# Kernel optimization log

Hardware: AMD Instinct MI355X
Metric: run time of the kernel (lower is better)

Reference implementation:

```python
import jax, jax.numpy as jnp
import numpy as np

REG_MAX = 16
TOPK = 13
ALPHA = 1.0
BETA = 6.0
MATCH_W = 0.5
IOU_W = 7.5
DFL_W = 1.5
EPS = 1e-7
NEG_INF = -1e30


def _iou(b1, b2):
    # xyxy IoU, broadcastable [..., 4]
    x1 = jnp.maximum(b1[..., 0], b2[..., 0]); y1 = jnp.maximum(b1[..., 1], b2[..., 1])
    x2 = jnp.minimum(b1[..., 2], b2[..., 2]); y2 = jnp.minimum(b1[..., 3], b2[..., 3])
    inter = jnp.maximum(x2 - x1, 0.0) * jnp.maximum(y2 - y1, 0.0)
    a1 = (b1[..., 2] - b1[..., 0]) * (b1[..., 3] - b1[..., 1])
    a2 = (b2[..., 2] - b2[..., 0]) * (b2[..., 3] - b2[..., 1])
    return inter / (a1 + a2 - inter + EPS)


def _ciou(b1, b2):
    iou = _iou(b1, b2)
    w1 = b1[..., 2] - b1[..., 0]; h1 = b1[..., 3] - b1[..., 1]
    w2 = b2[..., 2] - b2[..., 0]; h2 = b2[..., 3] - b2[..., 1]
    cw = jnp.maximum(b1[..., 2], b2[..., 2]) - jnp.minimum(b1[..., 0], b2[..., 0])
    ch = jnp.maximum(b1[..., 3], b2[..., 3]) - jnp.minimum(b1[..., 1], b2[..., 1])
    c2 = cw * cw + ch * ch + EPS
    rho2 = ((b2[..., 0] + b2[..., 2] - b1[..., 0] - b1[..., 2]) ** 2
            + (b2[..., 1] + b2[..., 3] - b1[..., 1] - b1[..., 3]) ** 2) / 4.0
    v = (4.0 / jnp.pi ** 2) * (jnp.arctan(w2 / (h2 + EPS)) - jnp.arctan(w1 / (h1 + EPS))) ** 2
    a = jax.lax.stop_gradient(v / (v - iou + (1.0 + EPS)))
    return iou - (rho2 / c2 + v * a)


def _per_sample(ps, pb, bd, gtb, gtl, vcm, anchor, stride):
    # ps [N,C], pb [N,4], bd [N,4*R], gtb [M,4], gtl [M], vcm [C] bool
    N, C = ps.shape
    M = gtb.shape[0]
    lab = jnp.clip(gtl, 0, C - 1)
    gt_valid = (gtl >= 0) & (gtl < C) & vcm[lab]
    ax, ay = anchor[:, 0], anchor[:, 1]
    inside = ((ax[None, :] >= gtb[:, 0:1]) & (ax[None, :] <= gtb[:, 2:3])
              & (ay[None, :] >= gtb[:, 1:2]) & (ay[None, :] <= gtb[:, 3:4]))  # [M,N]
    iou_mn = _iou(pb[None, :, :], gtb[:, None, :])                             # [M,N]
    cls_mn = jax.nn.sigmoid(ps[:, lab]).T                                      # [M,N]
    align = jnp.where(inside & gt_valid[:, None], cls_mn ** ALPHA * iou_mn ** BETA, NEG_INF)
    top_vals, top_idx = jax.lax.top_k(align, TOPK)                             # [M,K]
    cand = jnp.full((M, N), NEG_INF, ps.dtype).at[jnp.arange(M)[:, None], top_idx].set(top_vals)
    best = cand.max(0)          # final metric per anchor
    mg = cand.argmax(0)         # winning GT (first max == earliest GT, matching loop order)
    fg = best > -1.0            # align >= 0 always; non-candidates stay at NEG_INF
    m_lab = jnp.clip(gtl[mg], 0, C - 1)
    ov = iou_mn[mg, jnp.arange(N)]
    fgf = fg.astype(ps.dtype)
    tgt_scores = jax.nn.one_hot(m_lab, C, dtype=ps.dtype) * (jnp.maximum(ov, 0.1) * fgf)[:, None]
    tb = jnp.where(fg[:, None], gtb[mg], pb)   # safe target boxes (masked out when not fg)

    # classification BCE over valid classes (mean)
    bce = jnp.maximum(ps, 0.0) - ps * tgt_scores + jnp.log1p(jnp.exp(-jnp.abs(ps)))
    vc = vcm.astype(ps.dtype)
    match = (bce * vc[None, :]).sum() / (N * jnp.maximum(vc.sum(), 1.0))

    cnt = fg.sum()
    ciou_v = _ciou(pb, tb)
    iou_loss = jnp.where(cnt > 0, ((1.0 - ciou_v) * fgf).sum() / jnp.maximum(cnt, 1), 0.0)
    miou_sum = (_iou(pb, tb) * fgf).sum()
    probs = jax.nn.sigmoid(ps)
    pos_sum = (probs[jnp.arange(N), m_lab] * fgf).sum()

    # DFL
    d = jnp.concatenate([anchor - tb[:, :2], tb[:, 2:] - anchor], -1) / stride  # [N,4]
    d = jnp.clip(d, 0.0, REG_MAX - 1 - 0.01)
    tl = d.astype(jnp.int32)
    tr = jnp.minimum(tl + 1, REG_MAX - 1)
    wl = tr.astype(ps.dtype) - d
    wr = 1.0 - wl
    logp = jax.nn.log_softmax(bd.reshape(N, 4, REG_MAX), -1)
    ll = -jnp.take_along_axis(logp, tl[..., None], -1)[..., 0]
    lr = -jnp.take_along_axis(logp, tr[..., None], -1)[..., 0]
    dfl = jnp.where(cnt > 0, ((ll * wl + lr * wr) * fgf[:, None]).sum() / jnp.maximum(cnt * 4, 1), 0.0)

    mx = jnp.where(vcm[None, :], probs, NEG_INF).max(-1)
    neg_sum = (mx * (1.0 - fgf)).sum()
    neg_cnt = N - cnt
    return match, iou_loss, dfl, cnt, neg_cnt, pos_sum, neg_sum, miou_sum


def setup_inputs() -> dict:
    key = jax.random.key(0)
    B, N, C, M, R = 16, 8400, 80, 64, REG_MAX
    ks = jax.random.split(key, 7)
    pts, sts = [], []
    for s in (8, 16, 32):
        n = 640 // s
        g = (np.arange(n) + 0.5) * s
        xv, yv = np.meshgrid(g, g)
        pts.append(np.stack([xv.ravel(), yv.ravel()], 1))
        sts.append(np.full((n * n, 1), s, np.float32))
    anchor_points = jnp.asarray(np.concatenate(pts).astype(np.float32))  # [8400,2]
    stride_tensor = jnp.asarray(np.concatenate(sts))                      # [8400,1]
    c = anchor_points[None] + jax.random.normal(ks[0], (B, N, 2)) * stride_tensor[None]
    wh = jax.random.uniform(ks[1], (B, N, 2), minval=8.0, maxval=128.0)
    pred_boxes = jnp.concatenate([jnp.clip(c - wh / 2, 0.0, 640.0),
                                  jnp.clip(c + wh / 2, 0.0, 640.0)], -1)
    gc = jax.random.uniform(ks[2], (B, M, 2), minval=64.0, maxval=576.0)
    gwh = jax.random.uniform(ks[3], (B, M, 2), minval=16.0, maxval=128.0)
    gt_boxes = jnp.concatenate([gc - gwh / 2, gc + gwh / 2], -1)
    gt_labels = jax.random.randint(ks[4], (B, M), 0, C)
    class_mask = jnp.ones((B, C), bool)
    pred_scores = jax.random.normal(ks[5], (B, N, C))
    box_distribution = jax.random.normal(ks[6], (B, N, 4 * R))
    return {"pred_scores": pred_scores, "pred_boxes": pred_boxes,
            "anchor_points": anchor_points, "stride_tensor": stride_tensor,
            "box_distribution": box_distribution, "gt_boxes": gt_boxes,
            "gt_labels": gt_labels, "class_mask": class_mask}


def reference(pred_scores, pred_boxes, anchor_points, stride_tensor,
              box_distribution, gt_boxes, gt_labels, class_mask):
    B = pred_scores.shape[0]
    f = lambda ps, pb, bd, gtb, gtl, vcm: _per_sample(ps, pb, bd, gtb, gtl, vcm,
                                                      anchor_points, stride_tensor)
    match, iou_l, dfl, cnt, ncnt, psum, nsum, misum = jax.vmap(f)(
        pred_scores, pred_boxes, box_distribution, gt_boxes, gt_labels, class_mask)
    tot_pos = cnt.sum()
    tot_neg = ncnt.sum()
    total_match = match.sum(); total_iou = iou_l.sum(); total_dfl = dfl.sum()
    loss = (MATCH_W * total_match + IOU_W * total_iou + DFL_W * total_dfl) / B
    mean_pos = psum.sum() / jnp.maximum(tot_pos, 1)
    mean_neg = nsum.sum() / jnp.maximum(tot_neg, 1)
    mean_miou = misum.sum() / jnp.maximum(tot_pos, 1)
    return (loss, total_match / B, total_iou / B, total_dfl / B,
            tot_pos.astype(jnp.float32), mean_pos, mean_neg, mean_miou)
```

## Files before the change

kernel.cpp:

```cpp
#include <hip/hip_runtime.h>
#include <stdint.h>

#define TOPK 13
#define NEG_INF_F (-1e30f)
#define EPSF 1e-7f
#define L2EF 1.4426950408889634f
#define LN2F 0.6931471805599453f
#define MAXCAND 2048

__device__ __forceinline__ int mask_at(const uint8_t* __restrict__ raw, int i) {
    bool as_u8 = (raw[1] | raw[2] | raw[3]) != 0;
    return as_u8 ? (raw[i] != 0) : (((const int*)raw)[i] != 0);
}

__device__ __forceinline__ float iou_pair(float ax1, float ay1, float ax2, float ay2,
                                          float bx1, float by1, float bx2, float by2) {
    float x1 = fmaxf(ax1, bx1), y1 = fmaxf(ay1, by1);
    float x2 = fminf(ax2, bx2), y2 = fminf(ay2, by2);
    float inter = fmaxf(x2 - x1, 0.f) * fmaxf(y2 - y1, 0.f);
    float a1 = (ax2 - ax1) * (ay2 - ay1);
    float a2 = (bx2 - bx1) * (by2 - by1);
    return inter / (a1 + a2 - inter + EPSF);
}

__device__ __forceinline__ float sigmoid_fast(float s) {
    return 1.f / (1.f + exp2f(-s * L2EF));
}
__device__ __forceinline__ float softplus_bce(float s) {
    float t = exp2f(-fabsf(s) * L2EF);
    return fmaxf(s, 0.f) + log2f(1.f + t) * LN2F;
}

__global__ __launch_bounds__(64) void assign_grid_k(
    const float* __restrict__ ps, const float* __restrict__ pb,
    const float* __restrict__ gtb, const int* __restrict__ gtl,
    const uint8_t* __restrict__ mraw,
    unsigned long long* __restrict__ best, int B, int N, int C, int M) {
    int b = blockIdx.x % B;
    int m = blockIdx.x / B;

    int lbl = gtl[b * M + m];
    int lab = min(max(lbl, 0), C - 1);
    if (!((lbl >= 0) && (lbl < C) && (mask_at(mraw, b * C + lab) != 0))) return;

    float4 g = ((const float4*)gtb)[(size_t)b * M + m];

    const int   n0_[3]  = { 0, 6400, 8000 };
    const int   dim_[3] = { 80, 40, 20 };
    const float sv_[3]  = { 8.f, 16.f, 32.f };

    int ix0[3], iy0[3], ww[3], pre[4];
    pre[0] = 0;
#pragma unroll
    for (int l = 0; l < 3; ++l) {
        float s = sv_[l]; int d = dim_[l];
        int ax0 = max(0,     (int)ceilf (g.x / s - 0.5f));
        int ax1 = min(d - 1, (int)floorf(g.z / s - 0.5f));
        int ay0 = max(0,     (int)ceilf (g.y / s - 0.5f));
        int ay1 = min(d - 1, (int)floorf(g.w / s - 0.5f));
        int w = max(0, ax1 - ax0 + 1);
        int h = max(0, ay1 - ay0 + 1);
        ix0[l] = ax0; iy0[l] = ay0; ww[l] = w;
        pre[l + 1] = pre[l] + w * h;
    }
    int tot = pre[3];
    if (tot == 0) return;

    const float* psb = ps + (size_t)b * N * C + lab;
    const float4* pbb = (const float4*)pb + (size_t)b * N;
    int lane = threadIdx.x;

    float lv[TOPK];
    int   li[TOPK];
#pragma unroll
    for (int j = 0; j < TOPK; ++j) { lv[j] = NEG_INF_F; li[j] = -1; }

    for (int t = lane; t < tot; t += 64) {
        int l = (t >= pre[1]) + (t >= pre[2]);
        int r = t - pre[l];
        int w = ww[l];
        int iy = r / w, ix = r - iy * w;
        int gx = ix0[l] + ix, gy = iy0[l] + iy;
        int n = n0_[l] + gy * dim_[l] + gx;
        float4 p = pbb[n];
        float iou = iou_pair(p.x, p.y, p.z, p.w, g.x, g.y, g.z, g.w);
        float sc = psb[(size_t)n * C];
        float i3 = iou * iou * iou;
        float val = sigmoid_fast(sc) * i3 * i3;
        if (val > lv[TOPK - 1]) {
            bool placed = false;
#pragma unroll
            for (int j = TOPK - 1; j >= 1; --j) {
                if (!placed) {
                    if (val > lv[j - 1]) { lv[j] = lv[j - 1]; li[j] = li[j - 1]; }
                    else { lv[j] = val; li[j] = n; placed = true; }
                }
            }
            if (!placed) { lv[0] = val; li[0] = n; }
        }
    }

    unsigned key = 0xFFFFFFFFu - (unsigned)m;
    unsigned long long* bb = best + (size_t)b * N;
    int rounds = min(tot, TOPK);
    for (int p = 0; p < rounds; ++p) {
        float bv = lv[0]; int bn = li[0];
        for (int off = 32; off > 0; off >>= 1) {
            float ov = __shfl_down(bv, off, 64);
            int   on = __shfl_down(bn, off, 64);
            if (ov > bv || (ov == bv && (unsigned)on < (unsigned)bn)) { bv = ov; bn = on; }
        }
        bv = __shfl(bv, 0, 64);
        bn = __shfl(bn, 0, 64);
        if (bn < 0) break;
        if (li[0] == bn) {
            unsigned long long pk =
                ((unsigned long long)__float_as_uint(lv[0]) << 32) | (unsigned long long)key;
            atomicMax(bb + bn, pk);
#pragma unroll
            for (int j = 0; j < TOPK - 1; ++j) { lv[j] = lv[j + 1]; li[j] = li[j + 1]; }
            lv[TOPK - 1] = NEG_INF_F; li[TOPK - 1] = -1;
        }
    }
}

__global__ __launch_bounds__(256) void assign_topk_k(
    const float* __restrict__ ps, const float* __restrict__ pb,
    const float* __restrict__ anch, const float* __restrict__ gtb,
    const int* __restrict__ gtl, const uint8_t* __restrict__ mraw,
    unsigned long long* __restrict__ best, int B, int N, int C, int M) {
    int b = blockIdx.x % B;
    int m = blockIdx.x / B;

    __shared__ float cval[MAXCAND];
    __shared__ int   cidx[MAXCAND];
    __shared__ int   scnt;
    if (threadIdx.x == 0) scnt = 0;

    int lbl = gtl[b * M + m];
    int lab = min(max(lbl, 0), C - 1);
    bool valid = (lbl >= 0) && (lbl < C) && (mask_at(mraw, b * C + lab) != 0);
    __syncthreads();

    if (valid) {
        float4 g = ((const float4*)gtb)[(size_t)b * M + m];
        const float* psb = ps + (size_t)b * N * C + lab;
        const float4* pbb = (const float4*)pb + (size_t)b * N;
        for (int n = threadIdx.x; n < N; n += 256) {
            float2 a = ((const float2*)anch)[n];
            if (a.x < g.x || a.x > g.z || a.y < g.y || a.y > g.w) continue;
            float4 p = pbb[n];
            float iou = iou_pair(p.x, p.y, p.z, p.w, g.x, g.y, g.z, g.w);
            float s = psb[(size_t)n * C];
            float i3 = iou * iou * iou;
            float val = sigmoid_fast(s) * i3 * i3;
            int slot = atomicAdd(&scnt, 1);
            if (slot < MAXCAND) { cval[slot] = val; cidx[slot] = n; }
        }
    }
    __syncthreads();
    if (!valid || threadIdx.x >= 64) return;

    int total = min(scnt, MAXCAND);
    if (total == 0) return;
    int lane = threadIdx.x;

    float lv[TOPK];
    int   li[TOPK];
#pragma unroll
    for (int j = 0; j < TOPK; ++j) { lv[j] = NEG_INF_F; li[j] = -1; }
    for (int i = lane; i < total; i += 64) {
        float v = cval[i]; int ix = cidx[i];
        if (v > lv[TOPK - 1]) {
            bool placed = false;
#pragma unroll
            for (int j = TOPK - 1; j >= 1; --j) {
                if (!placed) {
                    if (v > lv[j - 1]) { lv[j] = lv[j - 1]; li[j] = li[j - 1]; }
                    else { lv[j] = v; li[j] = ix; placed = true; }
                }
            }
            if (!placed) { lv[0] = v; li[0] = ix; }
        }
    }

    unsigned key = 0xFFFFFFFFu - (unsigned)m;
    unsigned long long* bb = best + (size_t)b * N;
    int rounds = min(total, TOPK);
    for (int p = 0; p < rounds; ++p) {
        float bv = lv[0]; int bn = li[0];
        for (int off = 32; off > 0; off >>= 1) {
            float ov = __shfl_down(bv, off, 64);
            int   on = __shfl_down(bn, off, 64);
            if (ov > bv || (ov == bv && (unsigned)on < (unsigned)bn)) { bv = ov; bn = on; }
        }
        bv = __shfl(bv, 0, 64);
        bn = __shfl(bn, 0, 64);
        if (bn < 0) break;
        if (li[0] == bn) {
            unsigned long long pk =
                ((unsigned long long)__float_as_uint(lv[0]) << 32) | (unsigned long long)key;
            atomicMax(bb + bn, pk);
#pragma unroll
            for (int j = 0; j < TOPK - 1; ++j) { lv[j] = lv[j + 1]; li[j] = li[j + 1]; }
            lv[TOPK - 1] = NEG_INF_F; li[TOPK - 1] = -1;
        }
    }
}

__global__ __launch_bounds__(256, 1) void per_anchor_k(
    const float* __restrict__ ps, const float* __restrict__ pb,
    const float* __restrict__ anch, const float* __restrict__ strd,
    const float* __restrict__ bd, const float* __restrict__ gtb,
    const int* __restrict__ gtl, const uint8_t* __restrict__ mraw,
    const unsigned long long* __restrict__ best,
    float* __restrict__ partials, int B, int N, int C, int M) {
    int b = blockIdx.y;
    int n = blockIdx.x * 256 + threadIdx.x;

    __shared__ int smask[256];
    __shared__ int s_notall;
    __shared__ float sred[4 * 8];
    if (threadIdx.x == 0) s_notall = 0;
    __syncthreads();
    for (int c = threadIdx.x; c < C && c < 256; c += 256) {
        int v = mask_at(mraw, b * C + c);
        smask[c] = v;
        if (!v) s_notall = 1;
    }
    __syncthreads();
    bool allm = (s_notall == 0);

    float acc0 = 0, acc1 = 0, acc2 = 0, acc3 = 0, acc4 = 0, acc5 = 0, acc6 = 0;

    if (n < N) {
        unsigned long long pk = best[(size_t)b * N + n];
        bool fg = (pk != 0ull);
        int mg = fg ? (int)(0xFFFFFFFFu - (unsigned)(pk & 0xFFFFFFFFull)) : 0;
        int lbl = gtl[b * M + mg];
        int m_lab = min(max(lbl, 0), C - 1);

        const float* psr = ps + ((size_t)b * N + n) * C;
        float bce_sum = 0.f, smax = NEG_INF_F;

        if (C == 80 && allm) {
            const float4* p4 = (const float4*)psr;
            float4 s4[20];
#pragma unroll
            for (int i = 0; i < 20; ++i) s4[i] = p4[i];
#pragma unroll
            for (int i = 0; i < 20; ++i) {
                bce_sum += softplus_bce(s4[i].x) + softplus_bce(s4[i].y) +
                           softplus_bce(s4[i].z) + softplus_bce(s4[i].w);
                smax = fmaxf(smax, fmaxf(fmaxf(s4[i].x, s4[i].y), fmaxf(s4[i].z, s4[i].w)));
            }
        } else if (allm) {
            int c4 = C & ~3;
            for (int c = 0; c < c4; c += 4) {
                float4 s4 = *(const float4*)(psr + c);
                bce_sum += softplus_bce(s4.x) + softplus_bce(s4.y) +
                           softplus_bce(s4.z) + softplus_bce(s4.w);
                smax = fmaxf(smax, fmaxf(fmaxf(s4.x, s4.y), fmaxf(s4.z, s4.w)));
            }
            for (int c = c4; c < C; ++c) {
                float s = psr[c];
                bce_sum += softplus_bce(s);
                smax = fmaxf(smax, s);
            }
        } else {
            for (int c = 0; c < C; ++c) {
                float s = psr[c];
                if (smask[c]) { bce_sum += softplus_bce(s); smax = fmaxf(smax, s); }
            }
        }

        acc1 = fg ? 1.f : 0.f;
        acc3 = fg ? 0.f : sigmoid_fast(smax);

        if (fg) {
            const float* bdr = bd + ((size_t)b * N + n) * 64;
            const float4* bq4 = (const float4*)bdr;
            float4 bq[16];
#pragma unroll
            for (int i = 0; i < 16; ++i) bq[i] = bq4[i];
            float4 p = ((const float4*)pb)[(size_t)b * N + n];
            float4 g = ((const float4*)gtb)[(size_t)b * M + mg];
            float2 an = ((const float2*)anch)[n];
            float stv = strd[n];
            float slab = psr[m_lab];

            float ov = iou_pair(p.x, p.y, p.z, p.w, g.x, g.y, g.z, g.w);
            bce_sum -= fmaxf(ov, 0.1f) * slab;
            acc2 = sigmoid_fast(slab);
            acc4 = ov;
            float w1 = p.z - p.x, h1 = p.w - p.y;
            float w2 = g.z - g.x, h2 = g.w - g.y;
            float cw = fmaxf(p.z, g.z) - fminf(p.x, g.x);
            float ch = fmaxf(p.w, g.w) - fminf(p.y, g.y);
            float c2 = cw * cw + ch * ch + EPSF;
            float dx = g.x + g.z - p.x - p.z;
            float dy = g.y + g.w - p.y - p.w;
            float rho2 = (dx * dx + dy * dy) * 0.25f;
            const float PI = 3.14159265358979323846f;
            float dv = atanf(w2 / (h2 + EPSF)) - atanf(w1 / (h1 + EPSF));
            float v = (4.f / (PI * PI)) * dv * dv;
            float a = v / (v - ov + 1.f + EPSF);
            acc5 = 1.f - (ov - (rho2 / c2 + v * a));
            float dall[4] = { (an.x - g.x) / stv, (an.y - g.y) / stv,
                              (g.z - an.x) / stv, (g.w - an.y) / stv };
            float dfl = 0.f;
#pragma unroll
            for (int k = 0; k < 4; ++k) {
                float4 q0 = bq[k * 4 + 0], q1 = bq[k * 4 + 1];
                float4 q2 = bq[k * 4 + 2], q3 = bq[k * 4 + 3];
                float mxv = fmaxf(fmaxf(fmaxf(q0.x, q0.y), fmaxf(q0.z, q0.w)),
                                  fmaxf(fmaxf(q1.x, q1.y), fmaxf(q1.z, q1.w)));
                mxv = fmaxf(mxv, fmaxf(fmaxf(fmaxf(q2.x, q2.y), fmaxf(q2.z, q2.w)),
                                        fmaxf(fmaxf(q3.x, q3.y), fmaxf(q3.z, q3.w))));
                float se = exp2f((q0.x - mxv) * L2EF) + exp2f((q0.y - mxv) * L2EF) +
                           exp2f((q0.z - mxv) * L2EF) + exp2f((q0.w - mxv) * L2EF) +
                           exp2f((q1.x - mxv) * L2EF) + exp2f((q1.y - mxv) * L2EF) +
                           exp2f((q1.z - mxv) * L2EF) + exp2f((q1.w - mxv) * L2EF) +
                           exp2f((q2.x - mxv) * L2EF) + exp2f((q2.y - mxv) * L2EF) +
                           exp2f((q2.z - mxv) * L2EF) + exp2f((q2.w - mxv) * L2EF) +
                           exp2f((q3.x - mxv) * L2EF) + exp2f((q3.y - mxv) * L2EF) +
                           exp2f((q3.z - mxv) * L2EF) + exp2f((q3.w - mxv) * L2EF);
                float lse = mxv + log2f(se) * LN2F;
                float d = fminf(fmaxf(dall[k], 0.f), 14.99f);
                int tl = (int)d;
                int tr = min(tl + 1, 15);
                float wl = (float)tr - d;
                float xtl = bdr[k * 16 + tl];
                float xtr = bdr[k * 16 + tr];
                dfl += (lse - xtl) * wl + (lse - xtr) * (1.f - wl);
            }
            acc6 = dfl;
        }
        acc0 = bce_sum;
    }

    int lane = threadIdx.x & 63, wid = threadIdx.x >> 6;
    float accs[7] = { acc0, acc1, acc2, acc3, acc4, acc5, acc6 };
#pragma unroll
    for (int j = 0; j < 7; ++j) {
        float v = accs[j];
        for (int off = 32; off > 0; off >>= 1) v += __shfl_down(v, off, 64);
        if (lane == 0) sred[wid * 8 + j] = v;
    }
    __syncthreads();
    if (threadIdx.x < 7) {
        float s = sred[0 * 8 + threadIdx.x] + sred[1 * 8 + threadIdx.x] +
                  sred[2 * 8 + threadIdx.x] + sred[3 * 8 + threadIdx.x];
        atomicAdd(&partials[b * 8 + threadIdx.x], s);
    }
}

__global__ void finalize_k(const float* __restrict__ partials, const uint8_t* __restrict__ mraw,
                           float* __restrict__ out, int B, int N, int C) {
    int lane = threadIdx.x;
    float tm = 0, ti = 0, td = 0, tp = 0, tneg = 0, pos = 0, neg = 0, miou = 0;
    if (lane < B) {
        float vcs = 0.f;
        for (int c = 0; c < C; ++c) vcs += mask_at(mraw, lane * C + c) ? 1.f : 0.f;
        const float* pr = partials + lane * 8;
        float cnt = pr[1];
        tm = pr[0] / ((float)N * fmaxf(vcs, 1.f));
        ti = (cnt > 0.f) ? pr[5] / fmaxf(cnt, 1.f) : 0.f;
        td = (cnt > 0.f) ? pr[6] / fmaxf(cnt * 4.f, 1.f) : 0.f;
        tp = cnt; tneg = (float)N - cnt;
        pos = pr[2]; neg = pr[3]; miou = pr[4];
    }
    for (int off = 32; off > 0; off >>= 1) {
        tm += __shfl_down(tm, off, 64);   ti += __shfl_down(ti, off, 64);
        td += __shfl_down(td, off, 64);   tp += __shfl_down(tp, off, 64);
        tneg += __shfl_down(tneg, off, 64); pos += __shfl_down(pos, off, 64);
        neg += __shfl_down(neg, off, 64); miou += __shfl_down(miou, off, 64);
    }
    if (lane == 0) {
        float Bf = (float)B;
        out[0] = (0.5f * tm + 7.5f * ti + 1.5f * td) / Bf;
        out[1] = tm / Bf;
        out[2] = ti / Bf;
        out[3] = td / Bf;
        out[4] = tp;
        out[5] = pos / fmaxf(tp, 1.f);
        out[6] = neg / fmaxf(tneg, 1.f);
        out[7] = miou / fmaxf(tp, 1.f);
    }
}

extern "C" void kernel_launch(void* const* d_in, const int* in_sizes, int n_in,
                              void* d_out, int out_size, void* d_ws, size_t ws_size,
                              hipStream_t stream) {
    const float* ps   = (const float*)d_in[0];
    const float* pb   = (const float*)d_in[1];
    const float* anch = (const float*)d_in[2];
    const float* strd = (const float*)d_in[3];
    const float* bd   = (const float*)d_in[4];
    const float* gtb  = (const float*)d_in[5];
    const int*   gtl  = (const int*)d_in[6];
    const uint8_t* cmsk = (const uint8_t*)d_in[7];

    int N = in_sizes[2] / 2;
    int B = in_sizes[1] / (4 * N);
    int C = in_sizes[0] / (B * N);
    int M = in_sizes[6] / B;

    unsigned long long* best = (unsigned long long*)d_ws;
    size_t off = (size_t)B * N * sizeof(unsigned long long);
    off = (off + 255) & ~(size_t)255;
    float* partials = (float*)((char*)d_ws + off);
    size_t total = off + (size_t)B * 8 * sizeof(float);

    hipMemsetAsync(d_ws, 0, total, stream);
    if (N == 8400) {
        assign_grid_k<<<B * M, 64, 0, stream>>>(ps, pb, gtb, gtl, cmsk, best, B, N, C, M);
    } else {
        assign_topk_k<<<B * M, 256, 0, stream>>>(ps, pb, anch, gtb, gtl, cmsk, best, B, N, C, M);
    }
    dim3 gB((N + 255) / 256, B);
    per_anchor_k<<<gB, 256, 0, stream>>>(ps, pb, anch, strd, bd, gtb, gtl, cmsk, best,
                                         partials, B, N, C, M);
    finalize_k<<<1, 64, 0, stream>>>(partials, cmsk, (float*)d_out, B, N, C);
}
```

Baseline: 161.1 us.

## Overlap assignment with dense BCE pass and fold finalize into last block

For the N==8400 path, the per-GT assignment waves are packed four per 256-thread block. They run in the same launch as the dense per-anchor BCE/max pass, which does not depend on the assignment. The foreground-dependent terms move to a second kernel that reads the saved per-anchor max, and a last-block-done counter folds the finalize step into that kernel. This removes one launch and lets the assignment overlap the heavy class-score read, at the cost of an extra smax buffer round trip and a second pass over the foreground data.

```diff
diff --git a/kernel.cpp b/kernel.cpp
--- a/kernel.cpp
+++ b/kernel.cpp
@@ -31,13 +31,14 @@
     return fmaxf(s, 0.f) + log2f(1.f + t) * LN2F;
 }
 
-__global__ __launch_bounds__(64) void assign_grid_k(
+__device__ __forceinline__ void assign_wave(
     const float* __restrict__ ps, const float* __restrict__ pb,
     const float* __restrict__ gtb, const int* __restrict__ gtl,
     const uint8_t* __restrict__ mraw,
-    unsigned long long* __restrict__ best, int B, int N, int C, int M) {
-    int b = blockIdx.x % B;
-    int m = blockIdx.x / B;
+    unsigned long long* __restrict__ best, int B, int N, int C, int M,
+    int t, int lane) {
+    int b = t % B;
+    int m = t / B;
 
     int lbl = gtl[b * M + m];
     int lab = min(max(lbl, 0), C - 1);
@@ -68,16 +69,15 @@
 
     const float* psb = ps + (size_t)b * N * C + lab;
     const float4* pbb = (const float4*)pb + (size_t)b * N;
-    int lane = threadIdx.x;
 
     float lv[TOPK];
     int   li[TOPK];
 #pragma unroll
     for (int j = 0; j < TOPK; ++j) { lv[j] = NEG_INF_F; li[j] = -1; }
 
-    for (int t = lane; t < tot; t += 64) {
-        int l = (t >= pre[1]) + (t >= pre[2]);
-        int r = t - pre[l];
+    for (int tt = lane; tt < tot; tt += 64) {
+        int l = (tt >= pre[1]) + (tt >= pre[2]);
+        int r = tt - pre[l];
         int w = ww[l];
         int iy = r / w, ix = r - iy * w;
         int gx = ix0[l] + ix, gy = iy0[l] + iy;
@@ -124,103 +124,26 @@
     }
 }
 
-__global__ __launch_bounds__(256) void assign_topk_k(
+__global__ __launch_bounds__(256, 1) void fused_a_k(
     const float* __restrict__ ps, const float* __restrict__ pb,
-    const float* __restrict__ anch, const float* __restrict__ gtb,
-    const int* __restrict__ gtl, const uint8_t* __restrict__ mraw,
-    unsigned long long* __restrict__ best, int B, int N, int C, int M) {
-    int b = blockIdx.x % B;
-    int m = blockIdx.x / B;
-
-    __shared__ float cval[MAXCAND];
-    __shared__ int   cidx[MAXCAND];
-    __shared__ int   scnt;
-    if (threadIdx.x == 0) scnt = 0;
-
-    int lbl = gtl[b * M + m];
-    int lab = min(max(lbl, 0), C - 1);
-    bool valid = (lbl >= 0) && (lbl < C) && (mask_at(mraw, b * C + lab) != 0);
-    __syncthreads();
-
-    if (valid) {
-        float4 g = ((const float4*)gtb)[(size_t)b * M + m];
-        const float* psb = ps + (size_t)b * N * C + lab;
-        const float4* pbb = (const float4*)pb + (size_t)b * N;
-        for (int n = threadIdx.x; n < N; n += 256) {
-            float2 a = ((const float2*)anch)[n];
-            if (a.x < g.x || a.x > g.z || a.y < g.y || a.y > g.w) continue;
-            float4 p = pbb[n];
-            float iou = iou_pair(p.x, p.y, p.z, p.w, g.x, g.y, g.z, g.w);
-            float s = psb[(size_t)n * C];
-            float i3 = iou * iou * iou;
-            float val = sigmoid_fast(s) * i3 * i3;
-            int slot = atomicAdd(&scnt, 1);
-            if (slot < MAXCAND) { cval[slot] = val; cidx[slot] = n; }
-        }
-    }
-    __syncthreads();
-    if (!valid || threadIdx.x >= 64) return;
-
-    int total = min(scnt, MAXCAND);
-    if (total == 0) return;
-    int lane = threadIdx.x;
-
-    float lv[TOPK];
-    int   li[TOPK];
-#pragma unroll
-    for (int j = 0; j < TOPK; ++j) { lv[j] = NEG_INF_F; li[j] = -1; }
-    for (int i = lane; i < total; i += 64) {
-        float v = cval[i]; int ix = cidx[i];
-        if (v > lv[TOPK - 1]) {
-            bool placed = false;
-#pragma unroll
-            for (int j = TOPK - 1; j >= 1; --j) {
-                if (!placed) {
-                    if (v > lv[j - 1]) { lv[j] = lv[j - 1]; li[j] = li[j - 1]; }
-                    else { lv[j] = v; li[j] = ix; placed = true; }
-                }
-            }
-            if (!placed) { lv[0] = v; li[0] = ix; }
-        }
-    }
-
-    unsigned key = 0xFFFFFFFFu - (unsigned)m;
-    unsigned long long* bb = best + (size_t)b * N;
-    int rounds = min(total, TOPK);
-    for (int p = 0; p < rounds; ++p) {
-        float bv = lv[0]; int bn = li[0];
-        for (int off = 32; off > 0; off >>= 1) {
-            float ov = __shfl_down(bv, off, 64);
-            int   on = __shfl_down(bn, off, 64);
-            if (ov > bv || (ov == bv && (unsigned)on < (unsigned)bn)) { bv = ov; bn = on; }
-        }
-        bv = __shfl(bv, 0, 64);
-        bn = __shfl(bn, 0, 64);
-        if (bn < 0) break;
-        if (li[0] == bn) {
-            unsigned long long pk =
-                ((unsigned long long)__float_as_uint(lv[0]) << 32) | (unsigned long long)key;
-            atomicMax(bb + bn, pk);
-#pragma unroll
-            for (int j = 0; j < TOPK - 1; ++j) { lv[j] = lv[j + 1]; li[j] = li[j + 1]; }
-            lv[TOPK - 1] = NEG_INF_F; li[TOPK - 1] = -1;
-        }
-    }
-}
-
-__global__ __launch_bounds__(256, 1) void per_anchor_k(
-    const float* __restrict__ ps, const float* __restrict__ pb,
-    const float* __restrict__ anch, const float* __restrict__ strd,
-    const float* __restrict__ bd, const float* __restrict__ gtb,
-    const int* __restrict__ gtl, const uint8_t* __restrict__ mraw,
-    const unsigned long long* __restrict__ best,
-    float* __restrict__ partials, int B, int N, int C, int M) {
-    int b = blockIdx.y;
-    int n = blockIdx.x * 256 + threadIdx.x;
+    const float* __restrict__ gtb, const int* __restrict__ gtl,
+    const uint8_t* __restrict__ mraw,
+    unsigned long long* __restrict__ best, float* __restrict__ smaxbuf,
+    float* __restrict__ partials, int B, int N, int C, int M,
+    int asgb, int nb) {
+    if ((int)blockIdx.x < asgb) {
+        int t = blockIdx.x * 4 + (threadIdx.x >> 6);
+        if (t < B * M)
+            assign_wave(ps, pb, gtb, gtl, mraw, best, B, N, C, M, t, threadIdx.x & 63);
+        return;
+    }
+    int bi = blockIdx.x - asgb;
+    int b = bi / nb;
+    int n = (bi % nb) * 256 + threadIdx.x;
 
     __shared__ int smask[256];
     __shared__ int s_notall;
-    __shared__ float sred[4 * 8];
+    __shared__ float sredA[4];
     if (threadIdx.x == 0) s_notall = 0;
     __syncthreads();
     for (int c = threadIdx.x; c < C && c < 256; c += 256) {
@@ -231,15 +154,8 @@
     __syncthreads();
     bool allm = (s_notall == 0);
 
-    float acc0 = 0, acc1 = 0, acc2 = 0, acc3 = 0, acc4 = 0, acc5 = 0, acc6 = 0;
-
+    float acc0 = 0.f;
     if (n < N) {
-        unsigned long long pk = best[(size_t)b * N + n];
-        bool fg = (pk != 0ull);
-        int mg = fg ? (int)(0xFFFFFFFFu - (unsigned)(pk & 0xFFFFFFFFull)) : 0;
-        int lbl = gtl[b * M + mg];
-        int m_lab = min(max(lbl, 0), C - 1);
-
         const float* psr = ps + ((size_t)b * N + n) * C;
         float bce_sum = 0.f, smax = NEG_INF_F;
 
@@ -273,11 +189,47 @@
                 if (smask[c]) { bce_sum += softplus_bce(s); smax = fmaxf(smax, s); }
             }
         }
-
+        smaxbuf[(size_t)b * N + n] = smax;
+        acc0 = bce_sum;
+    }
+
+    int lane = threadIdx.x & 63, wid = threadIdx.x >> 6;
+    float v = acc0;
+    for (int off = 32; off > 0; off >>= 1) v += __shfl_down(v, off, 64);
+    if (lane == 0) sredA[wid] = v;
+    __syncthreads();
+    if (threadIdx.x == 0)
+        atomicAdd(&partials[b * 8 + 0], sredA[0] + sredA[1] + sredA[2] + sredA[3]);
+}
+
+__global__ __launch_bounds__(256, 1) void fused_b_k(
+    const float* __restrict__ ps, const float* __restrict__ pb,
+    const float* __restrict__ anch, const float* __restrict__ strd,
+    const float* __restrict__ bd, const float* __restrict__ gtb,
+    const int* __restrict__ gtl, const uint8_t* __restrict__ mraw,
+    const unsigned long long* __restrict__ best, const float* __restrict__ smaxbuf,
+    float* __restrict__ partials, unsigned int* __restrict__ done_ctr,
+    float* __restrict__ out, int B, int N, int C, int M) {
+    int b = blockIdx.y;
+    int n = blockIdx.x * 256 + threadIdx.x;
+
+    __shared__ float sred[4 * 8];
+    __shared__ int s_last;
+
+    float acc0 = 0, acc1 = 0, acc2 = 0, acc3 = 0, acc4 = 0, acc5 = 0, acc6 = 0;
+
+    if (n < N) {
+        unsigned long long pk = best[(size_t)b * N + n];
+        bool fg = (pk != 0ull);
+        float smax = smaxbuf[(size_t)b * N + n];
         acc1 = fg ? 1.f : 0.f;
         acc3 = fg ? 0.f : sigmoid_fast(smax);
 
         if (fg) {
+            int mg = (int)(0xFFFFFFFFu - (unsigned)(pk & 0xFFFFFFFFull));
+            int lbl = gtl[b * M + mg];
+            int m_lab = min(max(lbl, 0), C - 1);
+
             const float* bdr = bd + ((size_t)b * N + n) * 64;
             const float4* bq4 = (const float4*)bdr;
             float4 bq[16];
@@ -287,10 +239,10 @@
             float4 g = ((const float4*)gtb)[(size_t)b * M + mg];
             float2 an = ((const float2*)anch)[n];
             float stv = strd[n];
-            float slab = psr[m_lab];
+            float slab = ps[((size_t)b * N + n) * C + m_lab];
 
             float ov = iou_pair(p.x, p.y, p.z, p.w, g.x, g.y, g.z, g.w);
-            bce_sum -= fmaxf(ov, 0.1f) * slab;
+            acc0 = -fmaxf(ov, 0.1f) * slab;
             acc2 = sigmoid_fast(slab);
             acc4 = ov;
             float w1 = p.z - p.x, h1 = p.w - p.y;
@@ -336,6 +288,285 @@
             }
             acc6 = dfl;
         }
+    }
+
+    int lane = threadIdx.x & 63, wid = threadIdx.x >> 6;
+    float accs[7] = { acc0, acc1, acc2, acc3, acc4, acc5, acc6 };
+#pragma unroll
+    for (int j = 0; j < 7; ++j) {
+        float v = accs[j];
+        for (int off = 32; off > 0; off >>= 1) v += __shfl_down(v, off, 64);
+        if (lane == 0) sred[wid * 8 + j] = v;
+    }
+    __syncthreads();
+    if (threadIdx.x < 7) {
+        float s = sred[0 * 8 + threadIdx.x] + sred[1 * 8 + threadIdx.x] +
+                  sred[2 * 8 + threadIdx.x] + sred[3 * 8 + threadIdx.x];
+        atomicAdd(&partials[b * 8 + threadIdx.x], s);
+    }
+    __syncthreads();
+
+    if (threadIdx.x == 0) {
+        __threadfence();
+        unsigned r = atomicAdd(done_ctr, 1u);
+        s_last = (r == gridDim.x * gridDim.y - 1u) ? 1 : 0;
+    }
+    __syncthreads();
+    if (!s_last) return;
+    if (threadIdx.x >= 64) return;
+    __threadfence();
+
+    int fl = threadIdx.x;
+    float tm = 0, ti = 0, td = 0, tp = 0, tneg = 0, pos = 0, neg = 0, miou = 0;
+    for (int s = fl; s < B; s += 64) {
+        float vcs = 0.f;
+        for (int c = 0; c < C; ++c) vcs += mask_at(mraw, s * C + c) ? 1.f : 0.f;
+        const float* pr = partials + s * 8;
+        float p0 = __hip_atomic_load(&pr[0], __ATOMIC_RELAXED, __HIP_MEMORY_SCOPE_AGENT);
+        float p1 = __hip_atomic_load(&pr[1], __ATOMIC_RELAXED, __HIP_MEMORY_SCOPE_AGENT);
+        float p2 = __hip_atomic_load(&pr[2], __ATOMIC_RELAXED, __HIP_MEMORY_SCOPE_AGENT);
+        float p3 = __hip_atomic_load(&pr[3], __ATOMIC_RELAXED, __HIP_MEMORY_SCOPE_AGENT);
+        float p4 = __hip_atomic_load(&pr[4], __ATOMIC_RELAXED, __HIP_MEMORY_SCOPE_AGENT);
+        float p5 = __hip_atomic_load(&pr[5], __ATOMIC_RELAXED, __HIP_MEMORY_SCOPE_AGENT);
+        float p6 = __hip_atomic_load(&pr[6], __ATOMIC_RELAXED, __HIP_MEMORY_SCOPE_AGENT);
+        float cnt = p1;
+        tm += p0 / ((float)N * fmaxf(vcs, 1.f));
+        ti += (cnt > 0.f) ? p5 / fmaxf(cnt, 1.f) : 0.f;
+        td += (cnt > 0.f) ? p6 / fmaxf(cnt * 4.f, 1.f) : 0.f;
+        tp += cnt; tneg += (float)N - cnt;
+        pos += p2; neg += p3; miou += p4;
+    }
+    for (int off = 32; off > 0; off >>= 1) {
+        tm += __shfl_down(tm, off, 64);   ti += __shfl_down(ti, off, 64);
+        td += __shfl_down(td, off, 64);   tp += __shfl_down(tp, off, 64);
+        tneg += __shfl_down(tneg, off, 64); pos += __shfl_down(pos, off, 64);
+        neg += __shfl_down(neg, off, 64); miou += __shfl_down(miou, off, 64);
+    }
+    if (fl == 0) {
+        float Bf = (float)B;
+        out[0] = (0.5f * tm + 7.5f * ti + 1.5f * td) / Bf;
+        out[1] = tm / Bf;
+        out[2] = ti / Bf;
+        out[3] = td / Bf;
+        out[4] = tp;
+        out[5] = pos / fmaxf(tp, 1.f);
+        out[6] = neg / fmaxf(tneg, 1.f);
+        out[7] = miou / fmaxf(tp, 1.f);
+    }
+}
+
+__global__ __launch_bounds__(256) void assign_topk_k(
+    const float* __restrict__ ps, const float* __restrict__ pb,
+    const float* __restrict__ anch, const float* __restrict__ gtb,
+    const int* __restrict__ gtl, const uint8_t* __restrict__ mraw,
+    unsigned long long* __restrict__ best, int B, int N, int C, int M) {
+    int b = blockIdx.x % B;
+    int m = blockIdx.x / B;
+
+    __shared__ float cval[MAXCAND];
+    __shared__ int   cidx[MAXCAND];
+    __shared__ int   scnt;
+    if (threadIdx.x == 0) scnt = 0;
+
+    int lbl = gtl[b * M + m];
+    int lab = min(max(lbl, 0), C - 1);
+    bool valid = (lbl >= 0) && (lbl < C) && (mask_at(mraw, b * C + lab) != 0);
+    __syncthreads();
+
+    if (valid) {
+        float4 g = ((const float4*)gtb)[(size_t)b * M + m];
+        const float* psb = ps + (size_t)b * N * C + lab;
+        const float4* pbb = (const float4*)pb + (size_t)b * N;
+        for (int n = threadIdx.x; n < N; n += 256) {
+            float2 a = ((const float2*)anch)[n];
+            if (a.x < g.x || a.x > g.z || a.y < g.y || a.y > g.w) continue;
+            float4 p = pbb[n];
+            float iou = iou_pair(p.x, p.y, p.z, p.w, g.x, g.y, g.z, g.w);
+            float s = psb[(size_t)n * C];
+            float i3 = iou * iou * iou;
+            float val = sigmoid_fast(s) * i3 * i3;
+            int slot = atomicAdd(&scnt, 1);
+            if (slot < MAXCAND) { cval[slot] = val; cidx[slot] = n; }
+        }
+    }
+    __syncthreads();
+    if (!valid || threadIdx.x >= 64) return;
+
+    int total = min(scnt, MAXCAND);
+    if (total == 0) return;
+    int lane = threadIdx.x;
+
+    float lv[TOPK];
+    int   li[TOPK];
+#pragma unroll
+    for (int j = 0; j < TOPK; ++j) { lv[j] = NEG_INF_F; li[j] = -1; }
+    for (int i = lane; i < total; i += 64) {
+        float v = cval[i]; int ix = cidx[i];
+        if (v > lv[TOPK - 1]) {
+            bool placed = false;
+#pragma unroll
+            for (int j = TOPK - 1; j >= 1; --j) {
+                if (!placed) {
+                    if (v > lv[j - 1]) { lv[j] = lv[j - 1]; li[j] = li[j - 1]; }
+                    else { lv[j] = v; li[j] = ix; placed = true; }
+                }
+            }
+            if (!placed) { lv[0] = v; li[0] = ix; }
+        }
+    }
+
+    unsigned key = 0xFFFFFFFFu - (unsigned)m;
+    unsigned long long* bb = best + (size_t)b * N;
+    int rounds = min(total, TOPK);
+    for (int p = 0; p < rounds; ++p) {
+        float bv = lv[0]; int bn = li[0];
+        for (int off = 32; off > 0; off >>= 1) {
+            float ov = __shfl_down(bv, off, 64);
+            int   on = __shfl_down(bn, off, 64);
+            if (ov > bv || (ov == bv && (unsigned)on < (unsigned)bn)) { bv = ov; bn = on; }
+        }
+        bv = __shfl(bv, 0, 64);
+        bn = __shfl(bn, 0, 64);
+        if (bn < 0) break;
+        if (li[0] == bn) {
+            unsigned long long pk =
+                ((unsigned long long)__float_as_uint(lv[0]) << 32) | (unsigned long long)key;
+            atomicMax(bb + bn, pk);
+#pragma unroll
+            for (int j = 0; j < TOPK - 1; ++j) { lv[j] = lv[j + 1]; li[j] = li[j + 1]; }
+            lv[TOPK - 1] = NEG_INF_F; li[TOPK - 1] = -1;
+        }
+    }
+}
+
+__global__ __launch_bounds__(256, 1) void per_anchor_k(
+    const float* __restrict__ ps, const float* __restrict__ pb,
+    const float* __restrict__ anch, const float* __restrict__ strd,
+    const float* __restrict__ bd, const float* __restrict__ gtb,
+    const int* __restrict__ gtl, const uint8_t* __restrict__ mraw,
+    const unsigned long long* __restrict__ best,
+    float* __restrict__ partials, int B, int N, int C, int M) {
+    int b = blockIdx.y;
+    int n = blockIdx.x * 256 + threadIdx.x;
+
+    __shared__ int smask[256];
+    __shared__ int s_notall;
+    __shared__ float sred[4 * 8];
+    if (threadIdx.x == 0) s_notall = 0;
+    __syncthreads();
+    for (int c = threadIdx.x; c < C && c < 256; c += 256) {
+        int v = mask_at(mraw, b * C + c);
+        smask[c] = v;
+        if (!v) s_notall = 1;
+    }
+    __syncthreads();
+    bool allm = (s_notall == 0);
+
+    float acc0 = 0, acc1 = 0, acc2 = 0, acc3 = 0, acc4 = 0, acc5 = 0, acc6 = 0;
+
+    if (n < N) {
+        unsigned long long pk = best[(size_t)b * N + n];
+        bool fg = (pk != 0ull);
+        int mg = fg ? (int)(0xFFFFFFFFu - (unsigned)(pk & 0xFFFFFFFFull)) : 0;
+        int lbl = gtl[b * M + mg];
+        int m_lab = min(max(lbl, 0), C - 1);
+
+        const float* psr = ps + ((size_t)b * N + n) * C;
+        float bce_sum = 0.f, smax = NEG_INF_F;
+
+        if (C == 80 && allm) {
+            const float4* p4 = (const float4*)psr;
+            float4 s4[20];
+#pragma unroll
+            for (int i = 0; i < 20; ++i) s4[i] = p4[i];
+#pragma unroll
+            for (int i = 0; i < 20; ++i) {
+                bce_sum += softplus_bce(s4[i].x) + softplus_bce(s4[i].y) +
+                           softplus_bce(s4[i].z) + softplus_bce(s4[i].w);
+                smax = fmaxf(smax, fmaxf(fmaxf(s4[i].x, s4[i].y), fmaxf(s4[i].z, s4[i].w)));
+            }
+        } else if (allm) {
+            int c4 = C & ~3;
+            for (int c = 0; c < c4; c += 4) {
+                float4 s4 = *(const float4*)(psr + c);
+                bce_sum += softplus_bce(s4.x) + softplus_bce(s4.y) +
+                           softplus_bce(s4.z) + softplus_bce(s4.w);
+                smax = fmaxf(smax, fmaxf(fmaxf(s4.x, s4.y), fmaxf(s4.z, s4.w)));
+            }
+            for (int c = c4; c < C; ++c) {
+                float s = psr[c];
+                bce_sum += softplus_bce(s);
+                smax = fmaxf(smax, s);
+            }
+        } else {
+            for (int c = 0; c < C; ++c) {
+                float s = psr[c];
+                if (smask[c]) { bce_sum += softplus_bce(s); smax = fmaxf(smax, s); }
+            }
+        }
+
+        acc1 = fg ? 1.f : 0.f;
+        acc3 = fg ? 0.f : sigmoid_fast(smax);
+
+        if (fg) {
+            const float* bdr = bd + ((size_t)b * N + n) * 64;
+            const float4* bq4 = (const float4*)bdr;
+            float4 bq[16];
+#pragma unroll
+            for (int i = 0; i < 16; ++i) bq[i] = bq4[i];
+            float4 p = ((const float4*)pb)[(size_t)b * N + n];
+            float4 g = ((const float4*)gtb)[(size_t)b * M + mg];
+            float2 an = ((const float2*)anch)[n];
+            float stv = strd[n];
+            float slab = psr[m_lab];
+
+            float ov = iou_pair(p.x, p.y, p.z, p.w, g.x, g.y, g.z, g.w);
+            bce_sum -= fmaxf(ov, 0.1f) * slab;
+            acc2 = sigmoid_fast(slab);
+            acc4 = ov;
+            float w1 = p.z - p.x, h1 = p.w - p.y;
+            float w2 = g.z - g.x, h2 = g.w - g.y;
+            float cw = fmaxf(p.z, g.z) - fminf(p.x, g.x);
+            float ch = fmaxf(p.w, g.w) - fminf(p.y, g.y);
+            float c2 = cw * cw + ch * ch + EPSF;
+            float dx = g.x + g.z - p.x - p.z;
+            float dy = g.y + g.w - p.y - p.w;
+            float rho2 = (dx * dx + dy * dy) * 0.25f;
+            const float PI = 3.14159265358979323846f;
+            float dv = atanf(w2 / (h2 + EPSF)) - atanf(w1 / (h1 + EPSF));
+            float v = (4.f / (PI * PI)) * dv * dv;
+            float a = v / (v - ov + 1.f + EPSF);
+            acc5 = 1.f - (ov - (rho2 / c2 + v * a));
+            float dall[4] = { (an.x - g.x) / stv, (an.y - g.y) / stv,
+                              (g.z - an.x) / stv, (g.w - an.y) / stv };
+            float dfl = 0.f;
+#pragma unroll
+            for (int k = 0; k < 4; ++k) {
+                float4 q0 = bq[k * 4 + 0], q1 = bq[k * 4 + 1];
+                float4 q2 = bq[k * 4 + 2], q3 = bq[k * 4 + 3];
+                float mxv = fmaxf(fmaxf(fmaxf(q0.x, q0.y), fmaxf(q0.z, q0.w)),
+                                  fmaxf(fmaxf(q1.x, q1.y), fmaxf(q1.z, q1.w)));
+                mxv = fmaxf(mxv, fmaxf(fmaxf(fmaxf(q2.x, q2.y), fmaxf(q2.z, q2.w)),
+                                        fmaxf(fmaxf(q3.x, q3.y), fmaxf(q3.z, q3.w))));
+                float se = exp2f((q0.x - mxv) * L2EF) + exp2f((q0.y - mxv) * L2EF) +
+                           exp2f((q0.z - mxv) * L2EF) + exp2f((q0.w - mxv) * L2EF) +
+                           exp2f((q1.x - mxv) * L2EF) + exp2f((q1.y - mxv) * L2EF) +
+                           exp2f((q1.z - mxv) * L2EF) + exp2f((q1.w - mxv) * L2EF) +
+                           exp2f((q2.x - mxv) * L2EF) + exp2f((q2.y - mxv) * L2EF) +
+                           exp2f((q2.z - mxv) * L2EF) + exp2f((q2.w - mxv) * L2EF) +
+                           exp2f((q3.x - mxv) * L2EF) + exp2f((q3.y - mxv) * L2EF) +
+                           exp2f((q3.z - mxv) * L2EF) + exp2f((q3.w - mxv) * L2EF);
+                float lse = mxv + log2f(se) * LN2F;
+                float d = fminf(fmaxf(dall[k], 0.f), 14.99f);
+                int tl = (int)d;
+                int tr = min(tl + 1, 15);
+                float wl = (float)tr - d;
+                float xtl = bdr[k * 16 + tl];
+                float xtr = bdr[k * 16 + tr];
+                dfl += (lse - xtl) * wl + (lse - xtr) * (1.f - wl);
+            }
+            acc6 = dfl;
+        }
         acc0 = bce_sum;
     }
 
@@ -406,20 +637,32 @@
     int C = in_sizes[0] / (B * N);
     int M = in_sizes[6] / B;
 
+    size_t bestBytes = (size_t)B * N * sizeof(unsigned long long);
+    size_t off1 = (bestBytes + 255) & ~(size_t)255;
+    size_t partBytes = (size_t)B * 8 * sizeof(float);
+    size_t off2 = (off1 + partBytes + 255) & ~(size_t)255;
+    size_t zeroBytes = off2 + 256;
     unsigned long long* best = (unsigned long long*)d_ws;
-    size_t off = (size_t)B * N * sizeof(unsigned long long);
-    off = (off + 255) & ~(size_t)255;
-    float* partials = (float*)((char*)d_ws + off);
-    size_t total = off + (size_t)B * 8 * sizeof(float);
-
-    hipMemsetAsync(d_ws, 0, total, stream);
+    float* partials = (float*)((char*)d_ws + off1);
+    unsigned int* done_ctr = (unsigned int*)((char*)d_ws + off2);
+    float* smaxbuf = (float*)((char*)d_ws + zeroBytes);
+
+    hipMemsetAsync(d_ws, 0, zeroBytes, stream);
+
+    int nb = (N + 255) / 256;
     if (N == 8400) {
-        assign_grid_k<<<B * M, 64, 0, stream>>>(ps, pb, gtb, gtl, cmsk, best, B, N, C, M);
+        int asgb = (B * M + 3) / 4;
+        fused_a_k<<<asgb + B * nb, 256, 0, stream>>>(ps, pb, gtb, gtl, cmsk,
+                                                     best, smaxbuf, partials,
+                                                     B, N, C, M, asgb, nb);
+        fused_b_k<<<dim3(nb, B), 256, 0, stream>>>(ps, pb, anch, strd, bd, gtb, gtl, cmsk,
+                                                   best, smaxbuf, partials, done_ctr,
+                                                   (float*)d_out, B, N, C, M);
     } else {
         assign_topk_k<<<B * M, 256, 0, stream>>>(ps, pb, anch, gtb, gtl, cmsk, best, B, N, C, M);
-    }
-    dim3 gB((N + 255) / 256, B);
-    per_anchor_k<<<gB, 256, 0, stream>>>(ps, pb, anch, strd, bd, gtb, gtl, cmsk, best,
-                                         partials, B, N, C, M);
-    finalize_k<<<1, 64, 0, stream>>>(partials, cmsk, (float*)d_out, B, N, C);
-}
+        dim3 gB(nb, B);
+        per_anchor_k<<<gB, 256, 0, stream>>>(ps, pb, anch, strd, bd, gtb, gtl, cmsk, best,
+                                             partials, B, N, C, M);
+        finalize_k<<<1, 64, 0, stream>>>(partials, cmsk, (float*)d_out, B, N, C);
+    }
+}
```

After: 155.4 us. 3.5% less time.
